# Performance work log

Hardware: AMD Instinct MI355X
Metric: run time of the kernel (lower is better)

Reference implementation:

```python
import jax, jax.numpy as jnp
import numpy as np

N = 100000   # nodes
E = 3200000  # edges
F = 100      # raw node features
FE = 4       # feature_embed_dim
VE = 1       # value_embed_dim
D = F * (FE + VE)  # 500, embedded dim
H = 16
C = 40
EPS = 1e-5


def gcn_conv(x, edge_index, W, b, num_nodes):
    """PyG GCNConv: h = D^-1/2 (A+I) D^-1/2 (x W) + b."""
    loop = jnp.arange(num_nodes)
    src = jnp.concatenate([edge_index[0], loop])
    dst = jnp.concatenate([edge_index[1], loop])
    deg = jax.ops.segment_sum(jnp.ones_like(dst, dtype=x.dtype), dst,
                              num_segments=num_nodes)
    dinv = jnp.where(deg > 0, jax.lax.rsqrt(jnp.maximum(deg, 1e-12)), 0.0)
    norm = dinv[src] * dinv[dst]                      # [E+N]
    h = x @ W                                         # [N, out]
    msg = h[src] * norm[:, None]                      # gather + scale
    out = jax.ops.segment_sum(msg, dst, num_segments=num_nodes)
    return out + b


def setup_inputs() -> dict:
    key = jax.random.key(0)
    ks = jax.random.split(key, 10)
    x = jax.random.normal(ks[0], (N, F), dtype=jnp.float32)
    edge_index = jax.random.randint(ks[1], (2, E), 0, N, dtype=jnp.int64)
    feat_emb = jax.random.normal(ks[2], (F, FE), dtype=jnp.float32) * 0.1
    val_emb = jax.random.normal(ks[3], (F, VE), dtype=jnp.float32) * 0.1
    gamma = jnp.ones((D,), dtype=jnp.float32)
    beta = jnp.zeros((D,), dtype=jnp.float32)
    W1 = jax.random.normal(ks[4], (D, H), dtype=jnp.float32) * (1.0 / np.sqrt(D))
    b1 = jnp.zeros((H,), dtype=jnp.float32)
    W2 = jax.random.normal(ks[5], (H, C), dtype=jnp.float32) * (1.0 / np.sqrt(H))
    b2 = jnp.zeros((C,), dtype=jnp.float32)
    return {"x": x, "edge_index": edge_index, "feat_emb": feat_emb,
            "val_emb": val_emb, "gamma": gamma, "beta": beta,
            "W1": W1, "b1": b1, "W2": W2, "b2": b2}


def reference(x, edge_index, feat_emb, val_emb, gamma, beta, W1, b1, W2, b2):
    # embed_features: each scalar feature j -> x_ij * [e_j (4d), v_j (1d)]
    emb = jnp.concatenate([feat_emb, val_emb], axis=1)       # [F, 5]
    h = (x[:, :, None] * emb[None, :, :]).reshape(N, D)      # [N, 500]
    # BatchNorm1d (training-mode batch statistics)
    mean = jnp.mean(h, axis=0)
    var = jnp.mean(jnp.square(h - mean), axis=0)
    h = (h - mean) * jax.lax.rsqrt(var + EPS) * gamma + beta
    # conv1 -> relu (dropout is identity in eval)
    h = gcn_conv(h, edge_index, W1, b1, N)
    h = jax.nn.relu(h)
    # conv2 -> log_softmax
    h = gcn_conv(h, edge_index, W2, b2, N)
    return jax.nn.log_softmax(h, axis=1)
```

## Files before the change

kernel.cpp:

```cpp
#include <hip/hip_runtime.h>
#include <hip/hip_bf16.h>
#include <hip/hip_fp16.h>
#include <math.h>

#define N_NODES 100000
#define N_EDGES 3200000
#define F_IN    100
#define D_DIM   500
#define H_DIM   16
#define C_DIM   40
#define EPS_BN  1e-5f
#define PAD     72
#define NBUCK   196
#define BCKCAP  17408

#define WS_SUMS    0
#define WS_DEGI    256
#define WS_WX      100256
#define WS_C1      101856
#define WS_GCUR    101888
#define WS_DINV    102144
#define WS_BINNED  202240
#define WS_Y1      202240
#define WS_H1      1002240
#define WS_SSRC    3614208

#define MIX_STATS_BLOCKS 400
#define BIN_I4 512
#define NB_BIN 1563
#define MIX_BLOCKS (MIX_STATS_BLOCKS + NB_BIN)

__global__ void k_init(float* __restrict__ sums, int* __restrict__ gcur) {
    int t = threadIdx.x;
    sums[t] = 0.f;
    if (t < NBUCK) gcur[t] = t * BCKCAP;
}

__global__ void k_mixA(const float* __restrict__ x, const int* __restrict__ src,
                       const int* __restrict__ dst, float* __restrict__ sums,
                       int* __restrict__ gcur, int* __restrict__ binned) {
    __shared__ int smem[2816];
    if (blockIdx.x < MIX_STATS_BLOCKS) {
        float* ls = (float*)smem;
        for (int i = threadIdx.x; i < 200; i += 256) ls[i] = 0.f;
        __syncthreads();
        const int total4 = N_NODES * F_IN / 4;
        const float4* x4 = (const float4*)x;
        int g0 = blockIdx.x * 256 + threadIdx.x;
        int c0 = (4 * g0) % 100;
        float s0=0,s1=0,s2=0,s3=0,q0=0,q1=0,q2=0,q3=0;
        for (int g = g0; g < total4; g += MIX_STATS_BLOCKS * 256) {
            float4 v = x4[g];
            s0 += v.x; q0 += v.x*v.x;
            s1 += v.y; q1 += v.y*v.y;
            s2 += v.z; q2 += v.z*v.z;
            s3 += v.w; q3 += v.w*v.w;
        }
        atomicAdd(&ls[c0+0], s0); atomicAdd(&ls[100+c0+0], q0);
        atomicAdd(&ls[c0+1], s1); atomicAdd(&ls[100+c0+1], q1);
        atomicAdd(&ls[c0+2], s2); atomicAdd(&ls[100+c0+2], q2);
        atomicAdd(&ls[c0+3], s3); atomicAdd(&ls[100+c0+3], q3);
        __syncthreads();
        for (int i = threadIdx.x; i < 200; i += 256) {
            if (i < 100) atomicAdd(&sums[i], ls[i]);
            else         atomicAdd(&sums[128 + (i-100)], ls[i]);
        }
    } else {
        int* dstl = smem;
        int* cnt  = smem + 2048;
        int* base = smem + 2304;
        int* cnt2 = smem + 2560;
        int bb = blockIdx.x - MIX_STATS_BLOCKS;
        int t  = threadIdx.x;
        cnt[t] = 0; cnt2[t] = 0;
        __syncthreads();
        const int4* dst4 = (const int4*)dst;
        const int4* src4 = (const int4*)src;
        const int ne4 = N_EDGES / 4;
        int i40 = bb * BIN_I4;
        #pragma unroll
        for (int k = 0; k < 2; k++) {
            int i4 = i40 + t + 256 * k;
            if (i4 < ne4) {
                int4 d4 = dst4[i4];
                ((int4*)dstl)[t + 256 * k] = d4;
                atomicAdd(&cnt[d4.x >> 9], 1);
                atomicAdd(&cnt[d4.y >> 9], 1);
                atomicAdd(&cnt[d4.z >> 9], 1);
                atomicAdd(&cnt[d4.w >> 9], 1);
            }
        }
        __syncthreads();
        if (t < NBUCK && cnt[t] > 0) base[t] = atomicAdd(&gcur[t], cnt[t]);
        __syncthreads();
        #pragma unroll
        for (int k = 0; k < 2; k++) {
            int i4 = i40 + t + 256 * k;
            if (i4 < ne4) {
                int4 d4 = ((int4*)dstl)[t + 256 * k];
                int4 s4 = src4[i4];
                int bx, r;
                bx = d4.x >> 9; r = atomicAdd(&cnt2[bx], 1);
                binned[base[bx] + r] = ((d4.x & 511) << 17) | s4.x;
                bx = d4.y >> 9; r = atomicAdd(&cnt2[bx], 1);
                binned[base[bx] + r] = ((d4.y & 511) << 17) | s4.y;
                bx = d4.z >> 9; r = atomicAdd(&cnt2[bx], 1);
                binned[base[bx] + r] = ((d4.z & 511) << 17) | s4.z;
                bx = d4.w >> 9; r = atomicAdd(&cnt2[bx], 1);
                binned[base[bx] + r] = ((d4.w & 511) << 17) | s4.w;
            }
        }
    }
}

__global__ void k_bucketfold(const int* __restrict__ binned, const int* __restrict__ gcur,
                             int* __restrict__ ssrc, int* __restrict__ degi,
                             float* __restrict__ dinv,
                             const float* __restrict__ sums, const float* __restrict__ fe,
                             const float* __restrict__ ve, const float* __restrict__ gamma,
                             const float* __restrict__ beta, const float* __restrict__ W1,
                             float* __restrict__ wx, float* __restrict__ c1) {
    __shared__ float smf[1272];
    int t = threadIdx.x;
    if (blockIdx.x < NBUCK) {
        int* cnt = (int*)smf;
        for (int i = t; i < 512; i += 256) cnt[i] = 0;
        __syncthreads();
        int b   = blockIdx.x;
        int lo  = b * 512;
        int beg = b * BCKCAP;
        int nb  = min(gcur[b] - beg, BCKCAP);
        for (int e = t; e < nb; e += 256) {
            int v  = binned[beg + e];
            int ld = v >> 17;
            int sv = v & 0x1FFFF;
            int p = atomicAdd(&cnt[ld], 1);
            if (p < PAD) ssrc[(lo + ld) * PAD + p] = sv;
        }
        __syncthreads();
        for (int ld = t; ld < 512; ld += 256) {
            int d = lo + ld;
            if (d < N_NODES) {
                int c = cnt[ld];
                degi[d] = c;
                dinv[d] = rsqrtf((float)(c + 1));
            }
        }
    } else {
        float* a  = smf;
        float* mt = smf + 500;
        float (*cacc)[17] = (float(*)[17])(smf + 1000);
        const float invN = 1.0f / (float)N_NODES;
        for (int d = t; d < D_DIM; d += 256) {
            int j = d / 5, k = d % 5;
            float e   = (k < 4) ? fe[j*4 + k] : ve[j];
            float mx  = sums[j] * invN;
            float msq = sums[128 + j] * invN;
            float varx = msq - mx * mx;
            float rstd = rsqrtf(e*e*varx + EPS_BN);
            float ad = rstd * gamma[d];
            a[d]  = ad * e;
            mt[d] = beta[d] - (e * mx) * ad;
        }
        __syncthreads();
        for (int q = t; q < F_IN * H_DIM; q += 256) {
            int j = q >> 4, c = q & 15;
            float s = 0.f;
            #pragma unroll
            for (int k = 0; k < 5; k++) {
                int d = j*5 + k;
                s += a[d] * W1[d*16 + c];
            }
            wx[q] = s;
        }
        int c = t & 15, chunk = t >> 4;
        float s = 0.f;
        for (int d = chunk; d < D_DIM; d += 16) s += mt[d] * W1[d*16 + c];
        __syncthreads();
        cacc[chunk][c] = s;
        __syncthreads();
        if (t < 16) {
            float t2 = 0.f;
            #pragma unroll
            for (int q = 0; q < 16; q++) t2 += cacc[q][t];
            c1[t] = t2;
        }
    }
}

__global__ void k_y1(const float* __restrict__ x, const float* __restrict__ wx,
                     const float* __restrict__ c1, const float* __restrict__ dinv,
                     __half* __restrict__ y1s) {
    __shared__ float swx[F_IN * H_DIM];
    __shared__ float sx[16 * F_IN];
    __shared__ float sc1[16];
    int t = threadIdx.x;
    const float4* wx4 = (const float4*)wx;
    float4* swx4 = (float4*)swx;
    for (int i = t; i < 400; i += 256) swx4[i] = wx4[i];
    const float4* x4 = (const float4*)(x + blockIdx.x * 1600);
    float4* sx4 = (float4*)sx;
    for (int i = t; i < 400; i += 256) sx4[i] = x4[i];
    if (t < 16) sc1[t] = c1[t];
    __syncthreads();
    int ln = t >> 4, c = t & 15;
    int node = blockIdx.x * 16 + ln;
    const float* xr = sx + ln * F_IN;
    float s = sc1[c];
    #pragma unroll
    for (int j = 0; j < F_IN; j++) s += xr[j] * swx[j*16 + c];
    y1s[node * 16 + c] = __float2half(dinv[node] * s);
}

__global__ void k_agg1(const __half* __restrict__ y1s, const int* __restrict__ degi,
                       const int* __restrict__ ssrc, const float* __restrict__ dinv,
                       const float* __restrict__ b1, __half* __restrict__ h1s) {
    int g = blockIdx.x * 256 + threadIdx.x;
    int v = g >> 4, c = g & 15;
    int cnt = min(degi[v], PAD);
    const int4* s4p = (const int4*)(ssrc + v * PAD);
    float dv = dinv[v];
    float acc = __half2float(y1s[g]);
    int i = 0;
    for (; i + 8 <= cnt; i += 8) {
        int4 a4 = s4p[(i >> 2)];
        int4 b4 = s4p[(i >> 2) + 1];
        float t0 = __half2float(y1s[a4.x*16 + c]), t1 = __half2float(y1s[a4.y*16 + c]);
        float t2 = __half2float(y1s[a4.z*16 + c]), t3 = __half2float(y1s[a4.w*16 + c]);
        float t4 = __half2float(y1s[b4.x*16 + c]), t5 = __half2float(y1s[b4.y*16 + c]);
        float t6 = __half2float(y1s[b4.z*16 + c]), t7 = __half2float(y1s[b4.w*16 + c]);
        acc += ((t0 + t1) + (t2 + t3)) + ((t4 + t5) + (t6 + t7));
    }
    for (; i + 4 <= cnt; i += 4) {
        int4 a4 = s4p[(i >> 2)];
        float t0 = __half2float(y1s[a4.x*16 + c]), t1 = __half2float(y1s[a4.y*16 + c]);
        float t2 = __half2float(y1s[a4.z*16 + c]), t3 = __half2float(y1s[a4.w*16 + c]);
        acc += (t0 + t1) + (t2 + t3);
    }
    for (; i < cnt; i++) acc += __half2float(y1s[ssrc[v*PAD + i]*16 + c]);
    float tt = dv * acc + b1[c];
    h1s[g] = __float2half(dv * fmaxf(tt, 0.f));
}

__global__ void k_agg2f(const __half* __restrict__ h1s, const int* __restrict__ degi,
                        const int* __restrict__ ssrc, const float* __restrict__ dinv,
                        const float* __restrict__ b2, const float* __restrict__ W2,
                        float* __restrict__ out) {
    __shared__ float sw[H_DIM * C_DIM];
    __shared__ float sb[C_DIM];
    for (int i = threadIdx.x; i < H_DIM*C_DIM; i += 256) sw[i] = W2[i];
    if (threadIdx.x < C_DIM) sb[threadIdx.x] = b2[threadIdx.x];
    __syncthreads();
    int g = blockIdx.x * 256 + threadIdx.x;
    int v = g >> 4, c = g & 15;
    int cnt = min(degi[v], PAD);
    const int4* s4p = (const int4*)(ssrc + v * PAD);
    float acc = __half2float(h1s[g]);
    int i = 0;
    for (; i + 8 <= cnt; i += 8) {
        int4 a4 = s4p[(i >> 2)];
        int4 b4 = s4p[(i >> 2) + 1];
        float t0 = __half2float(h1s[a4.x*16 + c]), t1 = __half2float(h1s[a4.y*16 + c]);
        float t2 = __half2float(h1s[a4.z*16 + c]), t3 = __half2float(h1s[a4.w*16 + c]);
        float t4 = __half2float(h1s[b4.x*16 + c]), t5 = __half2float(h1s[b4.y*16 + c]);
        float t6 = __half2float(h1s[b4.z*16 + c]), t7 = __half2float(h1s[b4.w*16 + c]);
        acc += ((t0 + t1) + (t2 + t3)) + ((t4 + t5) + (t6 + t7));
    }
    for (; i + 4 <= cnt; i += 4) {
        int4 a4 = s4p[(i >> 2)];
        float t0 = __half2float(h1s[a4.x*16 + c]), t1 = __half2float(h1s[a4.y*16 + c]);
        float t2 = __half2float(h1s[a4.z*16 + c]), t3 = __half2float(h1s[a4.w*16 + c]);
        acc += (t0 + t1) + (t2 + t3);
    }
    for (; i < cnt; i++) acc += __half2float(h1s[ssrc[v*PAD + i]*16 + c]);
    float af = dinv[v] * acc;
    int lane = threadIdx.x & 63;
    int base = lane & ~15;
    float z0 = sb[c], z1 = sb[c+16];
    float z2 = (c < 8) ? sb[c+32] : 0.f;
    #pragma unroll
    for (int j = 0; j < 16; j++) {
        float aj = __shfl(af, base + j, 64);
        z0 += aj * sw[j*C_DIM + c];
        z1 += aj * sw[j*C_DIM + c + 16];
        if (c < 8) z2 += aj * sw[j*C_DIM + c + 32];
    }
    float m = fmaxf(z0, z1);
    if (c < 8) m = fmaxf(m, z2);
    #pragma unroll
    for (int off = 1; off < 16; off <<= 1) m = fmaxf(m, __shfl_xor(m, off, 64));
    float se = expf(z0 - m) + expf(z1 - m) + ((c < 8) ? expf(z2 - m) : 0.f);
    #pragma unroll
    for (int off = 1; off < 16; off <<= 1) se += __shfl_xor(se, off, 64);
    float lse = m + logf(se);
    float* orow = out + v * C_DIM;
    orow[c]      = z0 - lse;
    orow[c + 16] = z1 - lse;
    if (c < 8) orow[c + 32] = z2 - lse;
}

extern "C" void kernel_launch(void* const* d_in, const int* in_sizes, int n_in,
                              void* d_out, int out_size, void* d_ws, size_t ws_size,
                              hipStream_t stream) {
    const float* x     = (const float*)d_in[0];
    const int*   ei    = (const int*)d_in[1];
    const float* fe    = (const float*)d_in[2];
    const float* ve    = (const float*)d_in[3];
    const float* gamma = (const float*)d_in[4];
    const float* beta  = (const float*)d_in[5];
    const float* W1    = (const float*)d_in[6];
    const float* b1    = (const float*)d_in[7];
    const float* W2    = (const float*)d_in[8];
    const float* b2    = (const float*)d_in[9];
    float* out = (float*)d_out;

    float* wsf = (float*)d_ws;
    int*   wsi = (int*)d_ws;

    float*  sums   = wsf + WS_SUMS;
    int*    degi   = wsi + WS_DEGI;
    float*  wx     = wsf + WS_WX;
    float*  c1     = wsf + WS_C1;
    int*    gcur   = wsi + WS_GCUR;
    float*  dinv   = wsf + WS_DINV;
    int*    binned = wsi + WS_BINNED;
    int*    ssrc   = wsi + WS_SSRC;
    __half* y1s    = (__half*)(wsi + WS_Y1);
    __half* h1s    = (__half*)(wsi + WS_H1);

    const int* src = ei;
    const int* dst = ei + N_EDGES;

    k_init<<<1, 256, 0, stream>>>(sums, gcur);
    k_mixA<<<MIX_BLOCKS, 256, 0, stream>>>(x, src, dst, sums, gcur, binned);
    k_bucketfold<<<NBUCK + 1, 256, 0, stream>>>(binned, gcur, ssrc, degi, dinv,
                                                sums, fe, ve, gamma, beta, W1, wx, c1);
    k_y1<<<(N_NODES*H_DIM)/256, 256, 0, stream>>>(x, wx, c1, dinv, y1s);
    k_agg1<<<(N_NODES*H_DIM)/256, 256, 0, stream>>>(y1s, degi, ssrc, dinv, b1, h1s);
    k_agg2f<<<(N_NODES*H_DIM)/256, 256, 0, stream>>>(h1s, degi, ssrc, dinv, b2, W2, out);
}
```

Measured before the change: 294.2 us.

## Aggregate directly from destination buckets with shared-memory atomics, drop padded CSR

Removes the padded per-node source list (ssrc/degi) and the scatter that built it. Both GCN aggregation kernels now run one 1024-thread block per half-bucket: each block streams that bucket's binned edges, gathers 16-wide fp16 source rows, and accumulates into shared memory with atomics before applying the normalization, ReLU or the final linear layer plus log-softmax. The binning kernel also handles four int4 groups per block instead of two and guards bucket overflow. This cuts the bucketfold scatter traffic and the per-node degree cap. In exchange each aggregation block reads the whole bucket edge list and discards half of it, and relies on shared atomic throughput.

```diff
diff --git a/kernel.cpp b/kernel.cpp
--- a/kernel.cpp
+++ b/kernel.cpp
@@ -10,24 +10,20 @@
 #define H_DIM   16
 #define C_DIM   40
 #define EPS_BN  1e-5f
-#define PAD     72
 #define NBUCK   196
 #define BCKCAP  17408
 
 #define WS_SUMS    0
-#define WS_DEGI    256
-#define WS_WX      100256
-#define WS_C1      101856
-#define WS_GCUR    101888
-#define WS_DINV    102144
-#define WS_BINNED  202240
-#define WS_Y1      202240
-#define WS_H1      1002240
-#define WS_SSRC    3614208
+#define WS_WX      256
+#define WS_C1      1856
+#define WS_GCUR    1888
+#define WS_DINV    2144
+#define WS_BINNED  102400
+#define WS_Y1      3514368
+#define WS_H1      4314368
 
 #define MIX_STATS_BLOCKS 400
-#define BIN_I4 512
-#define NB_BIN 1563
+#define NB_BIN 782
 #define MIX_BLOCKS (MIX_STATS_BLOCKS + NB_BIN)
 
 __global__ void k_init(float* __restrict__ sums, int* __restrict__ gcur) {
@@ -39,7 +35,7 @@
 __global__ void k_mixA(const float* __restrict__ x, const int* __restrict__ src,
                        const int* __restrict__ dst, float* __restrict__ sums,
                        int* __restrict__ gcur, int* __restrict__ binned) {
-    __shared__ int smem[2816];
+    __shared__ int smem[4096 + 256 + 256 + 256];
     if (blockIdx.x < MIX_STATS_BLOCKS) {
         float* ls = (float*)smem;
         for (int i = threadIdx.x; i < 200; i += 256) ls[i] = 0.f;
@@ -67,9 +63,9 @@
         }
     } else {
         int* dstl = smem;
-        int* cnt  = smem + 2048;
-        int* base = smem + 2304;
-        int* cnt2 = smem + 2560;
+        int* cnt  = smem + 4096;
+        int* base = smem + 4352;
+        int* cnt2 = smem + 4608;
         int bb = blockIdx.x - MIX_STATS_BLOCKS;
         int t  = threadIdx.x;
         cnt[t] = 0; cnt2[t] = 0;
@@ -77,9 +73,9 @@
         const int4* dst4 = (const int4*)dst;
         const int4* src4 = (const int4*)src;
         const int ne4 = N_EDGES / 4;
-        int i40 = bb * BIN_I4;
+        int i40 = bb * 1024;
         #pragma unroll
-        for (int k = 0; k < 2; k++) {
+        for (int k = 0; k < 4; k++) {
             int i4 = i40 + t + 256 * k;
             if (i4 < ne4) {
                 int4 d4 = dst4[i4];
@@ -94,32 +90,31 @@
         if (t < NBUCK && cnt[t] > 0) base[t] = atomicAdd(&gcur[t], cnt[t]);
         __syncthreads();
         #pragma unroll
-        for (int k = 0; k < 2; k++) {
+        for (int k = 0; k < 4; k++) {
             int i4 = i40 + t + 256 * k;
             if (i4 < ne4) {
                 int4 d4 = ((int4*)dstl)[t + 256 * k];
                 int4 s4 = src4[i4];
-                int bx, r;
-                bx = d4.x >> 9; r = atomicAdd(&cnt2[bx], 1);
-                binned[base[bx] + r] = ((d4.x & 511) << 17) | s4.x;
-                bx = d4.y >> 9; r = atomicAdd(&cnt2[bx], 1);
-                binned[base[bx] + r] = ((d4.y & 511) << 17) | s4.y;
-                bx = d4.z >> 9; r = atomicAdd(&cnt2[bx], 1);
-                binned[base[bx] + r] = ((d4.z & 511) << 17) | s4.z;
-                bx = d4.w >> 9; r = atomicAdd(&cnt2[bx], 1);
-                binned[base[bx] + r] = ((d4.w & 511) << 17) | s4.w;
-            }
-        }
-    }
-}
-
-__global__ void k_bucketfold(const int* __restrict__ binned, const int* __restrict__ gcur,
-                             int* __restrict__ ssrc, int* __restrict__ degi,
-                             float* __restrict__ dinv,
-                             const float* __restrict__ sums, const float* __restrict__ fe,
-                             const float* __restrict__ ve, const float* __restrict__ gamma,
-                             const float* __restrict__ beta, const float* __restrict__ W1,
-                             float* __restrict__ wx, float* __restrict__ c1) {
+                int bx, r, adr;
+                bx = d4.x >> 9; r = atomicAdd(&cnt2[bx], 1); adr = base[bx] + r;
+                if (adr < (bx+1)*BCKCAP) binned[adr] = ((d4.x & 511) << 17) | s4.x;
+                bx = d4.y >> 9; r = atomicAdd(&cnt2[bx], 1); adr = base[bx] + r;
+                if (adr < (bx+1)*BCKCAP) binned[adr] = ((d4.y & 511) << 17) | s4.y;
+                bx = d4.z >> 9; r = atomicAdd(&cnt2[bx], 1); adr = base[bx] + r;
+                if (adr < (bx+1)*BCKCAP) binned[adr] = ((d4.z & 511) << 17) | s4.z;
+                bx = d4.w >> 9; r = atomicAdd(&cnt2[bx], 1); adr = base[bx] + r;
+                if (adr < (bx+1)*BCKCAP) binned[adr] = ((d4.w & 511) << 17) | s4.w;
+            }
+        }
+    }
+}
+
+__global__ void k_countfold(const int* __restrict__ binned, const int* __restrict__ gcur,
+                            float* __restrict__ dinv,
+                            const float* __restrict__ sums, const float* __restrict__ fe,
+                            const float* __restrict__ ve, const float* __restrict__ gamma,
+                            const float* __restrict__ beta, const float* __restrict__ W1,
+                            float* __restrict__ wx, float* __restrict__ c1) {
     __shared__ float smf[1272];
     int t = threadIdx.x;
     if (blockIdx.x < NBUCK) {
@@ -130,21 +125,12 @@
         int lo  = b * 512;
         int beg = b * BCKCAP;
         int nb  = min(gcur[b] - beg, BCKCAP);
-        for (int e = t; e < nb; e += 256) {
-            int v  = binned[beg + e];
-            int ld = v >> 17;
-            int sv = v & 0x1FFFF;
-            int p = atomicAdd(&cnt[ld], 1);
-            if (p < PAD) ssrc[(lo + ld) * PAD + p] = sv;
-        }
+        for (int e = t; e < nb; e += 256)
+            atomicAdd(&cnt[binned[beg + e] >> 17], 1);
         __syncthreads();
         for (int ld = t; ld < 512; ld += 256) {
             int d = lo + ld;
-            if (d < N_NODES) {
-                int c = cnt[ld];
-                degi[d] = c;
-                dinv[d] = rsqrtf((float)(c + 1));
-            }
+            if (d < N_NODES) dinv[d] = rsqrtf((float)(cnt[ld] + 1));
         }
     } else {
         float* a  = smf;
@@ -212,91 +198,158 @@
     y1s[node * 16 + c] = __float2half(dinv[node] * s);
 }
 
-__global__ void k_agg1(const __half* __restrict__ y1s, const int* __restrict__ degi,
-                       const int* __restrict__ ssrc, const float* __restrict__ dinv,
-                       const float* __restrict__ b1, __half* __restrict__ h1s) {
-    int g = blockIdx.x * 256 + threadIdx.x;
-    int v = g >> 4, c = g & 15;
-    int cnt = min(degi[v], PAD);
-    const int4* s4p = (const int4*)(ssrc + v * PAD);
-    float dv = dinv[v];
-    float acc = __half2float(y1s[g]);
-    int i = 0;
-    for (; i + 8 <= cnt; i += 8) {
-        int4 a4 = s4p[(i >> 2)];
-        int4 b4 = s4p[(i >> 2) + 1];
-        float t0 = __half2float(y1s[a4.x*16 + c]), t1 = __half2float(y1s[a4.y*16 + c]);
-        float t2 = __half2float(y1s[a4.z*16 + c]), t3 = __half2float(y1s[a4.w*16 + c]);
-        float t4 = __half2float(y1s[b4.x*16 + c]), t5 = __half2float(y1s[b4.y*16 + c]);
-        float t6 = __half2float(y1s[b4.z*16 + c]), t7 = __half2float(y1s[b4.w*16 + c]);
-        acc += ((t0 + t1) + (t2 + t3)) + ((t4 + t5) + (t6 + t7));
-    }
-    for (; i + 4 <= cnt; i += 4) {
-        int4 a4 = s4p[(i >> 2)];
-        float t0 = __half2float(y1s[a4.x*16 + c]), t1 = __half2float(y1s[a4.y*16 + c]);
-        float t2 = __half2float(y1s[a4.z*16 + c]), t3 = __half2float(y1s[a4.w*16 + c]);
-        acc += (t0 + t1) + (t2 + t3);
-    }
-    for (; i < cnt; i++) acc += __half2float(y1s[ssrc[v*PAD + i]*16 + c]);
-    float tt = dv * acc + b1[c];
-    h1s[g] = __float2half(dv * fmaxf(tt, 0.f));
-}
-
-__global__ void k_agg2f(const __half* __restrict__ h1s, const int* __restrict__ degi,
-                        const int* __restrict__ ssrc, const float* __restrict__ dinv,
-                        const float* __restrict__ b2, const float* __restrict__ W2,
-                        float* __restrict__ out) {
+__global__ void __launch_bounds__(1024)
+k_aggA(const __half* __restrict__ y1s, const int* __restrict__ gcur,
+       const int* __restrict__ binned, const float* __restrict__ dinv,
+       const float* __restrict__ b1, __half* __restrict__ h1s) {
+    __shared__ float acc[256 * 17];
+    int t = threadIdx.x;
+    int bucket = blockIdx.x >> 1, half = blockIdx.x & 1;
+    int lo = bucket * 512 + half * 256;
+    if (t < 512) {
+        int dl = t >> 1, s = t & 1;
+        int v = lo + dl;
+        if (v < N_NODES) {
+            int4 rw = *(const int4*)(y1s + v*16 + s*8);
+            const __half2* h2 = (const __half2*)&rw;
+            #pragma unroll
+            for (int k = 0; k < 4; k++) {
+                float2 f2 = __half22float2(h2[k]);
+                acc[dl*17 + s*8 + 2*k]     = f2.x;
+                acc[dl*17 + s*8 + 2*k + 1] = f2.y;
+            }
+        } else {
+            #pragma unroll
+            for (int k = 0; k < 8; k++) acc[dl*17 + s*8 + k] = 0.f;
+        }
+    }
+    int beg = bucket * BCKCAP;
+    int nb  = min(gcur[bucket] - beg, BCKCAP);
+    __syncthreads();
+    int ei0 = t >> 1, s = t & 1;
+    int vnext = (ei0 < nb) ? binned[beg + ei0] : -1;
+    for (int base = 0; base < nb; base += 512) {
+        int v = vnext;
+        int ni = base + 512 + ei0;
+        vnext = (ni < nb) ? binned[beg + ni] : -1;
+        int dl = (v >> 17) - half * 256;
+        if ((unsigned)dl < 256u) {
+            int srcv = v & 0x1FFFF;
+            int4 rw = *(const int4*)(y1s + srcv*16 + s*8);
+            const __half2* h2 = (const __half2*)&rw;
+            #pragma unroll
+            for (int k = 0; k < 4; k++) {
+                float2 f2 = __half22float2(h2[k]);
+                atomicAdd(&acc[dl*17 + s*8 + 2*k],     f2.x);
+                atomicAdd(&acc[dl*17 + s*8 + 2*k + 1], f2.y);
+            }
+        }
+    }
+    __syncthreads();
+    if (t < 512) {
+        int dl = t >> 1, sd = t & 1;
+        int v = lo + dl;
+        if (v < N_NODES) {
+            float dv = dinv[v];
+            __half hs[8];
+            #pragma unroll
+            for (int k = 0; k < 8; k++) {
+                float tt = dv * acc[dl*17 + sd*8 + k] + b1[sd*8 + k];
+                hs[k] = __float2half(dv * fmaxf(tt, 0.f));
+            }
+            *(int4*)(h1s + v*16 + sd*8) = *(int4*)hs;
+        }
+    }
+}
+
+__global__ void __launch_bounds__(1024)
+k_aggB(const __half* __restrict__ h1s, const int* __restrict__ gcur,
+       const int* __restrict__ binned, const float* __restrict__ dinv,
+       const float* __restrict__ b2, const float* __restrict__ W2,
+       float* __restrict__ out) {
+    __shared__ float acc[256 * 17];
     __shared__ float sw[H_DIM * C_DIM];
     __shared__ float sb[C_DIM];
-    for (int i = threadIdx.x; i < H_DIM*C_DIM; i += 256) sw[i] = W2[i];
-    if (threadIdx.x < C_DIM) sb[threadIdx.x] = b2[threadIdx.x];
-    __syncthreads();
-    int g = blockIdx.x * 256 + threadIdx.x;
-    int v = g >> 4, c = g & 15;
-    int cnt = min(degi[v], PAD);
-    const int4* s4p = (const int4*)(ssrc + v * PAD);
-    float acc = __half2float(h1s[g]);
-    int i = 0;
-    for (; i + 8 <= cnt; i += 8) {
-        int4 a4 = s4p[(i >> 2)];
-        int4 b4 = s4p[(i >> 2) + 1];
-        float t0 = __half2float(h1s[a4.x*16 + c]), t1 = __half2float(h1s[a4.y*16 + c]);
-        float t2 = __half2float(h1s[a4.z*16 + c]), t3 = __half2float(h1s[a4.w*16 + c]);
-        float t4 = __half2float(h1s[b4.x*16 + c]), t5 = __half2float(h1s[b4.y*16 + c]);
-        float t6 = __half2float(h1s[b4.z*16 + c]), t7 = __half2float(h1s[b4.w*16 + c]);
-        acc += ((t0 + t1) + (t2 + t3)) + ((t4 + t5) + (t6 + t7));
-    }
-    for (; i + 4 <= cnt; i += 4) {
-        int4 a4 = s4p[(i >> 2)];
-        float t0 = __half2float(h1s[a4.x*16 + c]), t1 = __half2float(h1s[a4.y*16 + c]);
-        float t2 = __half2float(h1s[a4.z*16 + c]), t3 = __half2float(h1s[a4.w*16 + c]);
-        acc += (t0 + t1) + (t2 + t3);
-    }
-    for (; i < cnt; i++) acc += __half2float(h1s[ssrc[v*PAD + i]*16 + c]);
-    float af = dinv[v] * acc;
-    int lane = threadIdx.x & 63;
-    int base = lane & ~15;
-    float z0 = sb[c], z1 = sb[c+16];
-    float z2 = (c < 8) ? sb[c+32] : 0.f;
-    #pragma unroll
-    for (int j = 0; j < 16; j++) {
-        float aj = __shfl(af, base + j, 64);
-        z0 += aj * sw[j*C_DIM + c];
-        z1 += aj * sw[j*C_DIM + c + 16];
-        if (c < 8) z2 += aj * sw[j*C_DIM + c + 32];
-    }
-    float m = fmaxf(z0, z1);
-    if (c < 8) m = fmaxf(m, z2);
-    #pragma unroll
-    for (int off = 1; off < 16; off <<= 1) m = fmaxf(m, __shfl_xor(m, off, 64));
-    float se = expf(z0 - m) + expf(z1 - m) + ((c < 8) ? expf(z2 - m) : 0.f);
-    #pragma unroll
-    for (int off = 1; off < 16; off <<= 1) se += __shfl_xor(se, off, 64);
-    float lse = m + logf(se);
-    float* orow = out + v * C_DIM;
-    orow[c]      = z0 - lse;
-    orow[c + 16] = z1 - lse;
-    if (c < 8) orow[c + 32] = z2 - lse;
+    int t = threadIdx.x;
+    for (int i = t; i < H_DIM * C_DIM; i += 1024) sw[i] = W2[i];
+    if (t < C_DIM) sb[t] = b2[t];
+    int bucket = blockIdx.x >> 1, half = blockIdx.x & 1;
+    int lo = bucket * 512 + half * 256;
+    if (t < 512) {
+        int dl = t >> 1, s = t & 1;
+        int v = lo + dl;
+        if (v < N_NODES) {
+            int4 rw = *(const int4*)(h1s + v*16 + s*8);
+            const __half2* h2 = (const __half2*)&rw;
+            #pragma unroll
+            for (int k = 0; k < 4; k++) {
+                float2 f2 = __half22float2(h2[k]);
+                acc[dl*17 + s*8 + 2*k]     = f2.x;
+                acc[dl*17 + s*8 + 2*k + 1] = f2.y;
+            }
+        } else {
+            #pragma unroll
+            for (int k = 0; k < 8; k++) acc[dl*17 + s*8 + k] = 0.f;
+        }
+    }
+    int beg = bucket * BCKCAP;
+    int nb  = min(gcur[bucket] - beg, BCKCAP);
+    __syncthreads();
+    int ei0 = t >> 1, s = t & 1;
+    int vnext = (ei0 < nb) ? binned[beg + ei0] : -1;
+    for (int base = 0; base < nb; base += 512) {
+        int v = vnext;
+        int ni = base + 512 + ei0;
+        vnext = (ni < nb) ? binned[beg + ni] : -1;
+        int dl = (v >> 17) - half * 256;
+        if ((unsigned)dl < 256u) {
+            int srcv = v & 0x1FFFF;
+            int4 rw = *(const int4*)(h1s + srcv*16 + s*8);
+            const __half2* h2 = (const __half2*)&rw;
+            #pragma unroll
+            for (int k = 0; k < 4; k++) {
+                float2 f2 = __half22float2(h2[k]);
+                atomicAdd(&acc[dl*17 + s*8 + 2*k],     f2.x);
+                atomicAdd(&acc[dl*17 + s*8 + 2*k + 1], f2.y);
+            }
+        }
+    }
+    __syncthreads();
+    if (t < 512) {
+        int dl = t >> 1, sd = t & 1;
+        int v = lo + dl;
+        if (v < N_NODES) {
+            float dv = dinv[v];
+            float a[16];
+            #pragma unroll
+            for (int j = 0; j < 16; j++) a[j] = dv * acc[dl*17 + j];
+            float z[20];
+            float m = -INFINITY;
+            #pragma unroll
+            for (int q = 0; q < 20; q++) {
+                int c = sd * 20 + q;
+                float zz = sb[c];
+                #pragma unroll
+                for (int j = 0; j < 16; j++) zz += a[j] * sw[j*C_DIM + c];
+                z[q] = zz;
+                m = fmaxf(m, zz);
+            }
+            m = fmaxf(m, __shfl_xor(m, 1, 64));
+            float se = 0.f;
+            #pragma unroll
+            for (int q = 0; q < 20; q++) se += expf(z[q] - m);
+            se += __shfl_xor(se, 1, 64);
+            float lse = m + logf(se);
+            float4 o4;
+            float* orow = out + v * C_DIM + sd * 20;
+            #pragma unroll
+            for (int q4 = 0; q4 < 5; q4++) {
+                o4.x = z[q4*4+0] - lse; o4.y = z[q4*4+1] - lse;
+                o4.z = z[q4*4+2] - lse; o4.w = z[q4*4+3] - lse;
+                *(float4*)(orow + q4*4) = o4;
+            }
+        }
+    }
 }
 
 extern "C" void kernel_launch(void* const* d_in, const int* in_sizes, int n_in,
@@ -318,13 +371,11 @@
     int*   wsi = (int*)d_ws;
 
     float*  sums   = wsf + WS_SUMS;
-    int*    degi   = wsi + WS_DEGI;
     float*  wx     = wsf + WS_WX;
     float*  c1     = wsf + WS_C1;
     int*    gcur   = wsi + WS_GCUR;
     float*  dinv   = wsf + WS_DINV;
     int*    binned = wsi + WS_BINNED;
-    int*    ssrc   = wsi + WS_SSRC;
     __half* y1s    = (__half*)(wsi + WS_Y1);
     __half* h1s    = (__half*)(wsi + WS_H1);
 
@@ -333,9 +384,9 @@
 
     k_init<<<1, 256, 0, stream>>>(sums, gcur);
     k_mixA<<<MIX_BLOCKS, 256, 0, stream>>>(x, src, dst, sums, gcur, binned);
-    k_bucketfold<<<NBUCK + 1, 256, 0, stream>>>(binned, gcur, ssrc, degi, dinv,
-                                                sums, fe, ve, gamma, beta, W1, wx, c1);
+    k_countfold<<<NBUCK + 1, 256, 0, stream>>>(binned, gcur, dinv,
+                                               sums, fe, ve, gamma, beta, W1, wx, c1);
     k_y1<<<(N_NODES*H_DIM)/256, 256, 0, stream>>>(x, wx, c1, dinv, y1s);
-    k_agg1<<<(N_NODES*H_DIM)/256, 256, 0, stream>>>(y1s, degi, ssrc, dinv, b1, h1s);
-    k_agg2f<<<(N_NODES*H_DIM)/256, 256, 0, stream>>>(h1s, degi, ssrc, dinv, b2, W2, out);
-}
+    k_aggA<<<2*NBUCK, 1024, 0, stream>>>(y1s, gcur, binned, dinv, b1, h1s);
+    k_aggB<<<2*NBUCK, 1024, 0, stream>>>(h1s, gcur, binned, dinv, b2, W2, out);
+}
```

Result: slower. 876.1 us (+197.8%).
